# Kernel tuning notes

Hardware: AMD Instinct MI355X
Metric: run time of the kernel (lower is better)

Reference implementation:

```python
import jax, jax.numpy as jnp
import numpy as np

N = 262144
H = 256
R = 32


def setup_inputs() -> dict:
    key = jax.random.key(0)
    ks = jax.random.split(key, 16)
    s = 1.0 / np.sqrt(H)
    return {
        "x": jax.random.normal(ks[0], (N, 1), jnp.float32),
        "t": jax.random.uniform(ks[1], (N, 1), jnp.float32),
        "start_w": jax.random.normal(ks[2], (H, 2), jnp.float32) * 0.5,
        "start_b": jax.random.normal(ks[3], (H,), jnp.float32) * 0.1,
        "end_w": jax.random.normal(ks[4], (1, H), jnp.float32) * s,
        "end_b": jax.random.normal(ks[5], (1,), jnp.float32) * 0.1,
        "col_0": jax.random.normal(ks[6], (H, R), jnp.float32) * s,
        "col_1": jax.random.normal(ks[7], (H, R), jnp.float32) * s,
        "col_2": jax.random.normal(ks[8], (H, R), jnp.float32) * s,
        "row_0": jax.random.normal(ks[9], (H, R), jnp.float32) * s,
        "row_1": jax.random.normal(ks[10], (H, R), jnp.float32) * s,
        "row_2": jax.random.normal(ks[11], (H, R), jnp.float32) * s,
        "alpha_0": jax.random.normal(ks[12], (R,), jnp.float32),
        "alpha_1": jax.random.normal(ks[13], (R,), jnp.float32),
        "alpha_2": jax.random.normal(ks[14], (R,), jnp.float32),
    }


def reference(x, t, start_w, start_b, end_w, end_b,
              col_0, col_1, col_2, row_0, row_1, row_2,
              alpha_0, alpha_1, alpha_2):
    # inputs: [N,2] -> start Linear -> tanh
    inp = jnp.concatenate([x, t], axis=1)
    h = jnp.tanh(inp @ start_w.T + start_b)  # [N, H]
    # three low-rank blocks: h @ (col * diag(alpha)) @ row.T, then tanh.
    # col_basis @ diag(alpha) == col_basis * alpha[None, :] (column scaling)
    for col, row, alpha in ((col_0, row_0, alpha_0),
                            (col_1, row_1, alpha_1),
                            (col_2, row_2, alpha_2)):
        h = jnp.tanh((h @ (col * alpha)) @ row.T)  # [N,H]->[N,R]->[N,H]
    return h @ end_w.T + end_b  # [N, 1]
```

## Files before the change

kernel.cpp:

```cpp
#include <hip/hip_runtime.h>


typedef _Float16 half4_t __attribute__((ext_vector_type(4)));
typedef __fp16   fp16x2  __attribute__((ext_vector_type(2)));
typedef float    float4_t __attribute__((ext_vector_type(4)));

#define TANH_SCALE 2.885390081777927f
#define MFMA16 __builtin_amdgcn_mfma_f32_16x16x16f16

namespace {

struct alignas(16) Smem {
  half4_t ctf[3 * 16 * 2 * 64];
  half4_t rwf[3 * 16 * 2 * 64];
  float w0[256], w1[256], bb[256];
  float ew[256];
  float rsC[3 * 32];
};

__device__ __forceinline__ half4_t pack4(float4_t v) {
  union { fp16x2 f2[2]; half4_t h4; } u;
  u.f2[0] = __builtin_amdgcn_cvt_pkrtz(v.x, v.y);
  u.f2[1] = __builtin_amdgcn_cvt_pkrtz(v.z, v.w);
  return u.h4;
}

__device__ __forceinline__ float inv_pre(float y) {
  return __builtin_amdgcn_rcpf(__builtin_amdgcn_exp2f(y) + 1.0f);
}

__device__ __forceinline__ half4_t inv4(float4_t v) {
  float4_t r;
  r.x = inv_pre(v.x); r.y = inv_pre(v.y);
  r.z = inv_pre(v.z); r.w = inv_pre(v.w);
  return pack4(r);
}

__global__ __launch_bounds__(1024)
__attribute__((amdgpu_waves_per_eu(4, 4)))
void pinn_fused(
    const float* __restrict__ xg, const float* __restrict__ tg,
    const float* __restrict__ sw, const float* __restrict__ sb,
    const float* __restrict__ ewp, const float* __restrict__ ebp,
    const float* __restrict__ c0, const float* __restrict__ c1,
    const float* __restrict__ c2, const float* __restrict__ r0,
    const float* __restrict__ r1, const float* __restrict__ r2,
    const float* __restrict__ a0, const float* __restrict__ a1,
    const float* __restrict__ a2, float* __restrict__ out, int n)
{
  __shared__ Smem sm;
  const int tid = threadIdx.x;

  for (int e = tid; e < 3 * 16 * 2 * 64; e += 1024) {
    const int lane_ = e & 63;
    const int sel   = (e >> 6) & 1;
    const int t_    = (e >> 7) & 15;
    const int k_    = e >> 11;
    const int m_ = lane_ & 15, q_ = lane_ >> 4;
    const float* ck = (k_ == 0) ? c0 : (k_ == 1) ? c1 : c2;
    const float* rk = (k_ == 0) ? r0 : (k_ == 1) ? r1 : r2;
    const float* ak = (k_ == 0) ? a0 : (k_ == 1) ? a1 : a2;
    {
      const int r = sel * 16 + m_;
      const float av = ak[r] * -2.0f;
      const int j0 = 16 * t_ + 4 * q_;
      half4_t v;
      v.x = (_Float16)(ck[(j0 + 0) * 32 + r] * av);
      v.y = (_Float16)(ck[(j0 + 1) * 32 + r] * av);
      v.z = (_Float16)(ck[(j0 + 2) * 32 + r] * av);
      v.w = (_Float16)(ck[(j0 + 3) * 32 + r] * av);
      sm.ctf[e] = v;
    }
    {
      const int j = 16 * t_ + m_;
      const int rr = sel * 16 + 4 * q_;
      half4_t v;
      v.x = (_Float16)(rk[j * 32 + rr + 0] * TANH_SCALE);
      v.y = (_Float16)(rk[j * 32 + rr + 1] * TANH_SCALE);
      v.z = (_Float16)(rk[j * 32 + rr + 2] * TANH_SCALE);
      v.w = (_Float16)(rk[j * 32 + rr + 3] * TANH_SCALE);
      sm.rwf[e] = v;
    }
  }
  if (tid < 256) {
    sm.w0[tid] = sw[2 * tid] * TANH_SCALE;
    sm.w1[tid] = sw[2 * tid + 1] * TANH_SCALE;
    sm.bb[tid] = sb[tid] * TANH_SCALE;
    sm.ew[tid] = ewp[tid] * -2.0f;
  }
  __syncthreads();

  if (tid < 96) {
    const int k_ = tid >> 5, r = tid & 31;
    const int sel = r >> 4, mm = r & 15;
    float s = 0.0f;
    for (int t = 0; t < 16; ++t)
      for (int qq = 0; qq < 4; ++qq) {
        const half4_t v = sm.ctf[((k_ * 16 + t) * 2 + sel) * 64 + 16 * qq + mm];
        s += (float)v.x + (float)v.y + (float)v.z + (float)v.w;
      }
    sm.rsC[k_ * 32 + r] = -0.5f * s;
  }
  __syncthreads();

  const int wave = tid >> 6;
  const int lane = tid & 63;
  const int m = lane & 15;
  const int q = lane >> 4;
  const int wo = 4 * q;
  const float ebv = ebp[0];
  const int tiles = n >> 4;

  float ewsum = 0.0f;
  for (int t = 0; t < 16; ++t) {
    const float4_t e4 = *(const float4_t*)&sm.ew[t * 16 + wo];
    ewsum += e4.x + e4.y + e4.z + e4.w;
  }
  ewsum *= -0.5f;

  const float4_t z4 = {0.f, 0.f, 0.f, 0.f};

#pragma unroll 1
  for (int g = (blockIdx.x * 16 + wave) * 4; g < tiles; g += 16384) {
    float xm[4], tm[4];
#pragma unroll
    for (int s = 0; s < 4; ++s) {
      xm[s] = xg[(g + s) * 16 + m];
      tm[s] = tg[(g + s) * 16 + m];
    }

    const float4_t rs00 = *(const float4_t*)&sm.rsC[wo];
    const float4_t rs01 = *(const float4_t*)&sm.rsC[16 + wo];
    float4_t acc[4][2];
#pragma unroll
    for (int s = 0; s < 4; ++s) { acc[s][0] = rs00; acc[s][1] = rs01; }
    const half4_t* cp0 = &sm.ctf[lane];
#pragma unroll 1
    for (int t = 0; t < 16; ++t) {
      const int cb = t * 16 + wo;
      const float4_t w0v = *(const float4_t*)&sm.w0[cb];
      const float4_t w1v = *(const float4_t*)&sm.w1[cb];
      const float4_t bv  = *(const float4_t*)&sm.bb[cb];
      half4_t h[4];
#pragma unroll
      for (int s = 0; s < 4; ++s) {
        float4_t z;
        z.x = fmaf(xm[s], w0v.x, fmaf(tm[s], w1v.x, bv.x));
        z.y = fmaf(xm[s], w0v.y, fmaf(tm[s], w1v.y, bv.y));
        z.z = fmaf(xm[s], w0v.z, fmaf(tm[s], w1v.z, bv.z));
        z.w = fmaf(xm[s], w0v.w, fmaf(tm[s], w1v.w, bv.w));
        h[s] = inv4(z);
      }
      const half4_t cA = cp0[0], cB = cp0[64];
#pragma unroll
      for (int s = 0; s < 4; ++s) acc[s][0] = MFMA16(cA, h[s], acc[s][0], 0, 0, 0);
#pragma unroll
      for (int s = 0; s < 4; ++s) acc[s][1] = MFMA16(cB, h[s], acc[s][1], 0, 0, 0);
      cp0 += 128;
    }

#pragma unroll 1
    for (int k = 0; k < 2; ++k) {
      half4_t pf[4][2];
#pragma unroll
      for (int s = 0; s < 4; ++s) {
        pf[s][0] = pack4(acc[s][0]);
        pf[s][1] = pack4(acc[s][1]);
      }
      const float4_t rsA = *(const float4_t*)&sm.rsC[(k + 1) * 32 + wo];
      const float4_t rsB = *(const float4_t*)&sm.rsC[(k + 1) * 32 + 16 + wo];
      float4_t nn[4][2];
#pragma unroll
      for (int s = 0; s < 4; ++s) { nn[s][0] = rsA; nn[s][1] = rsB; }
      const half4_t* rp = &sm.rwf[k * 2048 + lane];
      const half4_t* cp = &sm.ctf[(k + 1) * 2048 + lane];
#pragma unroll 1
      for (int t = 0; t < 16; ++t) {
        const half4_t rA = rp[0], rB = rp[64];
        const half4_t cA = cp[0], cB = cp[64];
        float4_t u[4];
#pragma unroll
        for (int s = 0; s < 4; ++s) u[s] = MFMA16(rA, pf[s][0], z4, 0, 0, 0);
#pragma unroll
        for (int s = 0; s < 4; ++s) u[s] = MFMA16(rB, pf[s][1], u[s], 0, 0, 0);
        half4_t h[4];
#pragma unroll
        for (int s = 0; s < 4; ++s) h[s] = inv4(u[s]);
#pragma unroll
        for (int s = 0; s < 4; ++s) nn[s][0] = MFMA16(cA, h[s], nn[s][0], 0, 0, 0);
#pragma unroll
        for (int s = 0; s < 4; ++s) nn[s][1] = MFMA16(cB, h[s], nn[s][1], 0, 0, 0);
        rp += 128; cp += 128;
      }
#pragma unroll
      for (int s = 0; s < 4; ++s) { acc[s][0] = nn[s][0]; acc[s][1] = nn[s][1]; }
    }

    float ssum[4] = {ewsum, ewsum, ewsum, ewsum};
    {
      half4_t pf[4][2];
#pragma unroll
      for (int s = 0; s < 4; ++s) {
        pf[s][0] = pack4(acc[s][0]);
        pf[s][1] = pack4(acc[s][1]);
      }
      const half4_t* rp = &sm.rwf[2 * 2048 + lane];
#pragma unroll 1
      for (int t = 0; t < 16; ++t) {
        const half4_t rA = rp[0], rB = rp[64];
        const float4_t ev = *(const float4_t*)&sm.ew[t * 16 + wo];
        float4_t u[4];
#pragma unroll
        for (int s = 0; s < 4; ++s) u[s] = MFMA16(rA, pf[s][0], z4, 0, 0, 0);
#pragma unroll
        for (int s = 0; s < 4; ++s) u[s] = MFMA16(rB, pf[s][1], u[s], 0, 0, 0);
#pragma unroll
        for (int s = 0; s < 4; ++s) {
          ssum[s] = fmaf(ev.x, inv_pre(u[s].x), ssum[s]);
          ssum[s] = fmaf(ev.y, inv_pre(u[s].y), ssum[s]);
          ssum[s] = fmaf(ev.z, inv_pre(u[s].z), ssum[s]);
          ssum[s] = fmaf(ev.w, inv_pre(u[s].w), ssum[s]);
        }
        rp += 128;
      }
    }

#pragma unroll
    for (int s = 0; s < 4; ++s) {
      ssum[s] += __shfl_xor(ssum[s], 16);
      ssum[s] += __shfl_xor(ssum[s], 32);
    }
    if (lane < 16) {
#pragma unroll
      for (int s = 0; s < 4; ++s) out[(g + s) * 16 + m] = ssum[s] + ebv;
    }
  }
}

}

extern "C" void kernel_launch(void* const* d_in, const int* in_sizes, int n_in,
                              void* d_out, int out_size, void* d_ws, size_t ws_size,
                              hipStream_t stream) {
  const float* xg  = (const float*)d_in[0];
  const float* tg  = (const float*)d_in[1];
  const float* sw  = (const float*)d_in[2];
  const float* sb  = (const float*)d_in[3];
  const float* ewp = (const float*)d_in[4];
  const float* ebp = (const float*)d_in[5];
  const float* c0  = (const float*)d_in[6];
  const float* c1  = (const float*)d_in[7];
  const float* c2  = (const float*)d_in[8];
  const float* r0  = (const float*)d_in[9];
  const float* r1  = (const float*)d_in[10];
  const float* r2  = (const float*)d_in[11];
  const float* a0  = (const float*)d_in[12];
  const float* a1  = (const float*)d_in[13];
  const float* a2  = (const float*)d_in[14];
  float* outp = (float*)d_out;

  const int n = in_sizes[0];

  pinn_fused<<<256, 1024, 0, stream>>>(xg, tg, sw, sb, ewp, ebp,
                                       c0, c1, c2, r0, r1, r2, a0, a1, a2,
                                       outp, n);
}
```

Baseline: 139.2 us.

## Switch to 16x16x32 f16 MFMA with permuted K-dimension weight layout

Replaces the 16x16x16 f16 MFMA with the gfx950 16x16x32 f16 instruction throughout all four stages. The shared-memory weight tables are repacked into half8 fragments, with permuted hidden and rank index orders so that accumulator outputs can be packed straight into the wider operand without shuffles. This halves the MFMA instruction count and the number of fragment loads per tile. The cost is a more intricate index permutation, including a reordered end weight vector, which must exactly match the accumulator layout to stay correct.

```diff
diff --git a/kernel.cpp b/kernel.cpp
--- a/kernel.cpp
+++ b/kernel.cpp
@@ -1,18 +1,19 @@
 #include <hip/hip_runtime.h>
 
 
+typedef _Float16 half8_t __attribute__((ext_vector_type(8)));
 typedef _Float16 half4_t __attribute__((ext_vector_type(4)));
 typedef __fp16   fp16x2  __attribute__((ext_vector_type(2)));
 typedef float    float4_t __attribute__((ext_vector_type(4)));
 
 #define TANH_SCALE 2.885390081777927f
-#define MFMA16 __builtin_amdgcn_mfma_f32_16x16x16f16
+#define MFMA32 __builtin_amdgcn_mfma_f32_16x16x32_f16
 
 namespace {
 
 struct alignas(16) Smem {
-  half4_t ctf[3 * 16 * 2 * 64];
-  half4_t rwf[3 * 16 * 2 * 64];
+  half8_t ctf[3 * 8 * 2 * 64];
+  half8_t rwf[3 * 16 * 64];
   float w0[256], w1[256], bb[256];
   float ew[256];
   float rsC[3 * 32];
@@ -23,6 +24,12 @@
   u.f2[0] = __builtin_amdgcn_cvt_pkrtz(v.x, v.y);
   u.f2[1] = __builtin_amdgcn_cvt_pkrtz(v.z, v.w);
   return u.h4;
+}
+
+__device__ __forceinline__ half8_t combine8(half4_t lo, half4_t hi) {
+  union { half4_t h4[2]; half8_t h8; } u;
+  u.h4[0] = lo; u.h4[1] = hi;
+  return u.h8;
 }
 
 __device__ __forceinline__ float inv_pre(float y) {
@@ -51,42 +58,43 @@
   __shared__ Smem sm;
   const int tid = threadIdx.x;
 
-  for (int e = tid; e < 3 * 16 * 2 * 64; e += 1024) {
+  for (int e = tid; e < 3 * 8 * 2 * 64; e += 1024) {
     const int lane_ = e & 63;
     const int sel   = (e >> 6) & 1;
-    const int t_    = (e >> 7) & 15;
-    const int k_    = e >> 11;
+    const int T_    = (e >> 7) & 7;
+    const int k_    = e >> 10;
     const int m_ = lane_ & 15, q_ = lane_ >> 4;
     const float* ck = (k_ == 0) ? c0 : (k_ == 1) ? c1 : c2;
+    const float* ak = (k_ == 0) ? a0 : (k_ == 1) ? a1 : a2;
+    const int rp_ = 8 * (m_ >> 2) + (m_ & 3) + 4 * sel;
+    const float av = ak[rp_] * -2.0f;
+    const int h0 = 32 * T_ + 8 * q_;
+    half8_t v;
+#pragma unroll
+    for (int j = 0; j < 8; ++j)
+      v[j] = (_Float16)(ck[(h0 + j) * 32 + rp_] * av);
+    sm.ctf[e] = v;
+  }
+  for (int e = tid; e < 3 * 16 * 64; e += 1024) {
+    const int lane_ = e & 63;
+    const int tp    = (e >> 6) & 15;
+    const int k_    = e >> 10;
+    const int m_ = lane_ & 15, q_ = lane_ >> 4;
     const float* rk = (k_ == 0) ? r0 : (k_ == 1) ? r1 : r2;
-    const float* ak = (k_ == 0) ? a0 : (k_ == 1) ? a1 : a2;
-    {
-      const int r = sel * 16 + m_;
-      const float av = ak[r] * -2.0f;
-      const int j0 = 16 * t_ + 4 * q_;
-      half4_t v;
-      v.x = (_Float16)(ck[(j0 + 0) * 32 + r] * av);
-      v.y = (_Float16)(ck[(j0 + 1) * 32 + r] * av);
-      v.z = (_Float16)(ck[(j0 + 2) * 32 + r] * av);
-      v.w = (_Float16)(ck[(j0 + 3) * 32 + r] * av);
-      sm.ctf[e] = v;
-    }
-    {
-      const int j = 16 * t_ + m_;
-      const int rr = sel * 16 + 4 * q_;
-      half4_t v;
-      v.x = (_Float16)(rk[j * 32 + rr + 0] * TANH_SCALE);
-      v.y = (_Float16)(rk[j * 32 + rr + 1] * TANH_SCALE);
-      v.z = (_Float16)(rk[j * 32 + rr + 2] * TANH_SCALE);
-      v.w = (_Float16)(rk[j * 32 + rr + 3] * TANH_SCALE);
-      sm.rwf[e] = v;
-    }
+    const int hrow = 32 * (tp >> 1) + 8 * (m_ >> 2) + 4 * (tp & 1) + (m_ & 3);
+    half8_t v;
+#pragma unroll
+    for (int j = 0; j < 8; ++j)
+      v[j] = (_Float16)(rk[hrow * 32 + 8 * q_ + j] * TANH_SCALE);
+    sm.rwf[e] = v;
   }
   if (tid < 256) {
     sm.w0[tid] = sw[2 * tid] * TANH_SCALE;
     sm.w1[tid] = sw[2 * tid + 1] * TANH_SCALE;
     sm.bb[tid] = sb[tid] * TANH_SCALE;
-    sm.ew[tid] = ewp[tid] * -2.0f;
+    const int tp = tid >> 4, ii = tid & 15;
+    const int hph = 32 * (tp >> 1) + 8 * (ii >> 2) + 4 * (tp & 1) + (ii & 3);
+    sm.ew[tid] = ewp[hph] * -2.0f;
   }
   __syncthreads();
 
@@ -94,10 +102,13 @@
     const int k_ = tid >> 5, r = tid & 31;
     const int sel = r >> 4, mm = r & 15;
     float s = 0.0f;
-    for (int t = 0; t < 16; ++t)
+    for (int T = 0; T < 8; ++T)
       for (int qq = 0; qq < 4; ++qq) {
-        const half4_t v = sm.ctf[((k_ * 16 + t) * 2 + sel) * 64 + 16 * qq + mm];
-        s += (float)v.x + (float)v.y + (float)v.z + (float)v.w;
+        const half8_t v = sm.ctf[((k_ * 8 + T) * 2 + sel) * 64 + 16 * qq + mm];
+        float ps = 0.0f;
+#pragma unroll
+        for (int j = 0; j < 8; ++j) ps += (float)v[j];
+        s += ps;
       }
     sm.rsC[k_ * 32 + r] = -0.5f * s;
   }
@@ -108,6 +119,7 @@
   const int m = lane & 15;
   const int q = lane >> 4;
   const int wo = 4 * q;
+  const int wo8 = 8 * q;
   const float ebv = ebp[0];
   const int tiles = n >> 4;
 
@@ -134,62 +146,71 @@
     float4_t acc[4][2];
 #pragma unroll
     for (int s = 0; s < 4; ++s) { acc[s][0] = rs00; acc[s][1] = rs01; }
-    const half4_t* cp0 = &sm.ctf[lane];
-#pragma unroll 1
-    for (int t = 0; t < 16; ++t) {
-      const int cb = t * 16 + wo;
-      const float4_t w0v = *(const float4_t*)&sm.w0[cb];
-      const float4_t w1v = *(const float4_t*)&sm.w1[cb];
-      const float4_t bv  = *(const float4_t*)&sm.bb[cb];
-      half4_t h[4];
+    const half8_t* cp0 = &sm.ctf[lane];
+#pragma unroll 1
+    for (int T = 0; T < 8; ++T) {
+      const int cb = 32 * T + wo8;
+      const float4_t w0a = *(const float4_t*)&sm.w0[cb];
+      const float4_t w0b = *(const float4_t*)&sm.w0[cb + 4];
+      const float4_t w1a = *(const float4_t*)&sm.w1[cb];
+      const float4_t w1b = *(const float4_t*)&sm.w1[cb + 4];
+      const float4_t ba  = *(const float4_t*)&sm.bb[cb];
+      const float4_t bb2 = *(const float4_t*)&sm.bb[cb + 4];
+      half8_t h[4];
 #pragma unroll
       for (int s = 0; s < 4; ++s) {
-        float4_t z;
-        z.x = fmaf(xm[s], w0v.x, fmaf(tm[s], w1v.x, bv.x));
-        z.y = fmaf(xm[s], w0v.y, fmaf(tm[s], w1v.y, bv.y));
-        z.z = fmaf(xm[s], w0v.z, fmaf(tm[s], w1v.z, bv.z));
-        z.w = fmaf(xm[s], w0v.w, fmaf(tm[s], w1v.w, bv.w));
-        h[s] = inv4(z);
-      }
-      const half4_t cA = cp0[0], cB = cp0[64];
-#pragma unroll
-      for (int s = 0; s < 4; ++s) acc[s][0] = MFMA16(cA, h[s], acc[s][0], 0, 0, 0);
-#pragma unroll
-      for (int s = 0; s < 4; ++s) acc[s][1] = MFMA16(cB, h[s], acc[s][1], 0, 0, 0);
+        float4_t za, zb;
+        za.x = fmaf(xm[s], w0a.x, fmaf(tm[s], w1a.x, ba.x));
+        za.y = fmaf(xm[s], w0a.y, fmaf(tm[s], w1a.y, ba.y));
+        za.z = fmaf(xm[s], w0a.z, fmaf(tm[s], w1a.z, ba.z));
+        za.w = fmaf(xm[s], w0a.w, fmaf(tm[s], w1a.w, ba.w));
+        zb.x = fmaf(xm[s], w0b.x, fmaf(tm[s], w1b.x, bb2.x));
+        zb.y = fmaf(xm[s], w0b.y, fmaf(tm[s], w1b.y, bb2.y));
+        zb.z = fmaf(xm[s], w0b.z, fmaf(tm[s], w1b.z, bb2.z));
+        zb.w = fmaf(xm[s], w0b.w, fmaf(tm[s], w1b.w, bb2.w));
+        h[s] = combine8(inv4(za), inv4(zb));
+      }
+      const half8_t cA = cp0[0], cB = cp0[64];
+#pragma unroll
+      for (int s = 0; s < 4; ++s) acc[s][0] = MFMA32(cA, h[s], acc[s][0], 0, 0, 0);
+#pragma unroll
+      for (int s = 0; s < 4; ++s) acc[s][1] = MFMA32(cB, h[s], acc[s][1], 0, 0, 0);
       cp0 += 128;
     }
 
 #pragma unroll 1
     for (int k = 0; k < 2; ++k) {
-      half4_t pf[4][2];
-#pragma unroll
-      for (int s = 0; s < 4; ++s) {
-        pf[s][0] = pack4(acc[s][0]);
-        pf[s][1] = pack4(acc[s][1]);
-      }
+      half8_t pf[4];
+#pragma unroll
+      for (int s = 0; s < 4; ++s)
+        pf[s] = combine8(pack4(acc[s][0]), pack4(acc[s][1]));
       const float4_t rsA = *(const float4_t*)&sm.rsC[(k + 1) * 32 + wo];
       const float4_t rsB = *(const float4_t*)&sm.rsC[(k + 1) * 32 + 16 + wo];
       float4_t nn[4][2];
 #pragma unroll
       for (int s = 0; s < 4; ++s) { nn[s][0] = rsA; nn[s][1] = rsB; }
-      const half4_t* rp = &sm.rwf[k * 2048 + lane];
-      const half4_t* cp = &sm.ctf[(k + 1) * 2048 + lane];
-#pragma unroll 1
-      for (int t = 0; t < 16; ++t) {
-        const half4_t rA = rp[0], rB = rp[64];
-        const half4_t cA = cp[0], cB = cp[64];
-        float4_t u[4];
-#pragma unroll
-        for (int s = 0; s < 4; ++s) u[s] = MFMA16(rA, pf[s][0], z4, 0, 0, 0);
-#pragma unroll
-        for (int s = 0; s < 4; ++s) u[s] = MFMA16(rB, pf[s][1], u[s], 0, 0, 0);
-        half4_t h[4];
-#pragma unroll
-        for (int s = 0; s < 4; ++s) h[s] = inv4(u[s]);
-#pragma unroll
-        for (int s = 0; s < 4; ++s) nn[s][0] = MFMA16(cA, h[s], nn[s][0], 0, 0, 0);
-#pragma unroll
-        for (int s = 0; s < 4; ++s) nn[s][1] = MFMA16(cB, h[s], nn[s][1], 0, 0, 0);
+      const half8_t* rp = &sm.rwf[k * 1024 + lane];
+      const half8_t* cp = &sm.ctf[(k + 1) * 1024 + lane];
+#pragma unroll 1
+      for (int t2 = 0; t2 < 8; ++t2) {
+        const half8_t rA = rp[0], rB = rp[64];
+        const half8_t cA = cp[0], cB = cp[64];
+        float4_t u0[4];
+#pragma unroll
+        for (int s = 0; s < 4; ++s) u0[s] = MFMA32(rA, pf[s], z4, 0, 0, 0);
+        half4_t hl[4];
+#pragma unroll
+        for (int s = 0; s < 4; ++s) hl[s] = inv4(u0[s]);
+        float4_t u1[4];
+#pragma unroll
+        for (int s = 0; s < 4; ++s) u1[s] = MFMA32(rB, pf[s], z4, 0, 0, 0);
+        half8_t h[4];
+#pragma unroll
+        for (int s = 0; s < 4; ++s) h[s] = combine8(hl[s], inv4(u1[s]));
+#pragma unroll
+        for (int s = 0; s < 4; ++s) nn[s][0] = MFMA32(cA, h[s], nn[s][0], 0, 0, 0);
+#pragma unroll
+        for (int s = 0; s < 4; ++s) nn[s][1] = MFMA32(cB, h[s], nn[s][1], 0, 0, 0);
         rp += 128; cp += 128;
       }
 #pragma unroll
@@ -198,22 +219,18 @@
 
     float ssum[4] = {ewsum, ewsum, ewsum, ewsum};
     {
-      half4_t pf[4][2];
-#pragma unroll
-      for (int s = 0; s < 4; ++s) {
-        pf[s][0] = pack4(acc[s][0]);
-        pf[s][1] = pack4(acc[s][1]);
-      }
-      const half4_t* rp = &sm.rwf[2 * 2048 + lane];
-#pragma unroll 1
-      for (int t = 0; t < 16; ++t) {
-        const half4_t rA = rp[0], rB = rp[64];
-        const float4_t ev = *(const float4_t*)&sm.ew[t * 16 + wo];
+      half8_t pf[4];
+#pragma unroll
+      for (int s = 0; s < 4; ++s)
+        pf[s] = combine8(pack4(acc[s][0]), pack4(acc[s][1]));
+      const half8_t* rp = &sm.rwf[2 * 1024 + lane];
+#pragma unroll 1
+      for (int tp = 0; tp < 16; ++tp) {
+        const half8_t rA = rp[0];
+        const float4_t ev = *(const float4_t*)&sm.ew[tp * 16 + wo];
         float4_t u[4];
 #pragma unroll
-        for (int s = 0; s < 4; ++s) u[s] = MFMA16(rA, pf[s][0], z4, 0, 0, 0);
-#pragma unroll
-        for (int s = 0; s < 4; ++s) u[s] = MFMA16(rB, pf[s][1], u[s], 0, 0, 0);
+        for (int s = 0; s < 4; ++s) u[s] = MFMA32(rA, pf[s], z4, 0, 0, 0);
 #pragma unroll
         for (int s = 0; s < 4; ++s) {
           ssum[s] = fmaf(ev.x, inv_pre(u[s].x), ssum[s]);
@@ -221,7 +238,7 @@
           ssum[s] = fmaf(ev.z, inv_pre(u[s].z), ssum[s]);
           ssum[s] = fmaf(ev.w, inv_pre(u[s].w), ssum[s]);
         }
-        rp += 128;
+        rp += 64;
       }
     }
 
```

New measurement: 138.0 us. About the same (-0.9%).
